# Performance work log

Measured on AMD Instinct MI355X. Metric: run time of the kernel, lower is better.

## Reference

```python
import jax, jax.numpy as jnp
import numpy as np

N, FIN, FOUT = 4096, 512, 256
ALPHA = 0.2          # LeakyReLU negative slope
NEG_INF = -9e15      # mask value from the torch source


def setup_inputs() -> dict:
    key = jax.random.key(0)
    ks = jax.random.split(key, 11)
    h = jax.random.normal(ks[0], (N, FIN), dtype=jnp.float32)
    adj_n = jax.random.randint(ks[1], (N, N), 0, 2, dtype=jnp.int32)
    adj_d = jax.random.randint(ks[2], (N, N), 0, 2, dtype=jnp.int32)
    G_nd = jax.random.normal(ks[3], (2, N, FOUT), dtype=jnp.float32)
    # learned parameters (xavier-ish scale)
    W_n = jax.random.normal(ks[4], (FIN, FOUT), dtype=jnp.float32) * 0.05
    a1_n = jax.random.normal(ks[5], (FOUT, 1), dtype=jnp.float32) * 0.05
    a2_n = jax.random.normal(ks[6], (FOUT, 1), dtype=jnp.float32) * 0.05
    W_d = jax.random.normal(ks[7], (FIN, FOUT), dtype=jnp.float32) * 0.05
    a1_d = jax.random.normal(ks[8], (FOUT, 1), dtype=jnp.float32) * 0.05
    a2_d = jax.random.normal(ks[9], (FOUT, 1), dtype=jnp.float32) * 0.05
    scale = jnp.zeros((1,), dtype=jnp.float32)
    return {"h": h, "adj_n": adj_n, "adj_d": adj_d, "G_nd": G_nd,
            "W_n": W_n, "a1_n": a1_n, "a2_n": a2_n,
            "W_d": W_d, "a1_d": a1_d, "a2_d": a2_d, "scale": scale}


def _gat(h, adj, W, a1, a2):
    # Wh: [N, FOUT]
    Wh = h @ W
    # outer-sum attention logits: e[i,j] = leakyrelu(Wh_i.a1 + Wh_j.a2)
    e = jax.nn.leaky_relu((Wh @ a1) + (Wh @ a2).T, negative_slope=ALPHA)  # [N, N]
    att = jnp.where(adj > 0, e, jnp.float32(NEG_INF))
    att = jax.nn.softmax(att, axis=-1)
    # dropout is identity in eval mode
    return jax.nn.elu(att @ Wh)  # [N, FOUT]


def reference(h, adj_n, adj_d, G_nd, W_n, a1_n, a2_n, W_d, a1_d, a2_d, scale):
    f_n_S = _gat(h, adj_n, W_n, a1_n, a2_n)
    f_d_S = _gat(h, adj_d, W_d, a1_d, a2_d)
    # The G_nd cross-attention branch (f_nd_C) in the torch source is computed
    # but never used in the returned value; omitted here (jit would DCE it).
    return f_n_S + f_d_S
```

## Files before the change

kernel.cpp:

```cpp
#include <hip/hip_runtime.h>

#define N_NODES 4096
#define FIN     512
#define FOUT    256

typedef __attribute__((ext_vector_type(8))) short bf16x8s;
typedef __attribute__((ext_vector_type(4))) float f32x4;
typedef __attribute__((ext_vector_type(8))) unsigned short u16x8;
typedef unsigned short u16;
typedef unsigned int   u32;

__device__ inline u16 f2b(float f) {
    union { float f; unsigned int u; } v; v.f = f;
    unsigned int r = v.u + 0x7fffu + ((v.u >> 16) & 1u);
    return (u16)(r >> 16);
}

__global__ __launch_bounds__(256) void prep_kernel(
    const float* __restrict__ h, const float* __restrict__ Wn,
    const float* __restrict__ Wd,
    u16* __restrict__ hb, u16* __restrict__ WTb, float* __restrict__ s12)
{
    __shared__ u16 tl[64 * 72];
    const int t = threadIdx.x;
    const int bid = blockIdx.x;

    if (bid < 1024) {
        int idx = (bid * 256 + t) * 8;
        float4 f0 = *(const float4*)&h[idx];
        float4 f1 = *(const float4*)&h[idx + 4];
        u16x8 o;
        o[0]=f2b(f0.x); o[1]=f2b(f0.y); o[2]=f2b(f0.z); o[3]=f2b(f0.w);
        o[4]=f2b(f1.x); o[5]=f2b(f1.y); o[6]=f2b(f1.z); o[7]=f2b(f1.w);
        *(u16x8*)&hb[idx] = o;
    } else if (bid < 1088) {
        int id = bid - 1024;
        int kx = id & 7, ny = (id >> 3) & 3, b = id >> 5;
        const float* W = b ? Wd : Wn;
        int k0 = kx * 64, n0 = ny * 64;
        int kr = t >> 2, nc0 = (t & 3) * 16;
        const float* src = W + (size_t)(k0 + kr) * FOUT + n0 + nc0;
        #pragma unroll
        for (int jv = 0; jv < 4; ++jv) {
            float4 f = *(const float4*)(src + jv * 4);
            tl[(nc0 + jv * 4 + 0) * 72 + kr] = f2b(f.x);
            tl[(nc0 + jv * 4 + 1) * 72 + kr] = f2b(f.y);
            tl[(nc0 + jv * 4 + 2) * 72 + kr] = f2b(f.z);
            tl[(nc0 + jv * 4 + 3) * 72 + kr] = f2b(f.w);
        }
        __syncthreads();
        int n = t >> 2, kc0 = (t & 3) * 16;
        u16* dst = WTb + ((size_t)b << 17) + (size_t)(n0 + n) * FIN + k0 + kc0;
        *(uint4*)dst       = *(uint4*)&tl[n * 72 + kc0];
        *(uint4*)(dst + 8) = *(uint4*)&tl[n * 72 + kc0 + 8];
    } else {
        float4 z = {0.f, 0.f, 0.f, 0.f};
        float4* p4 = (float4*)s12;
        #pragma unroll
        for (int k = 0; k < 16; ++k) p4[k * 256 + t] = z;
    }
}

__global__ __launch_bounds__(256) void wh_gemm_kernel(
    const u16* __restrict__ hb, const u16* __restrict__ WTb,
    const float* __restrict__ a1n, const float* __restrict__ a2n,
    const float* __restrict__ a1d, const float* __restrict__ a2d,
    u16* __restrict__ WhT, float* __restrict__ s1, float* __restrict__ s2)
{
    __shared__ u16 smem[8192];
    u16* a_lds = smem;
    u16* b_lds = smem + 4096;

    const int t = threadIdx.x, lane = t & 63, w = t >> 6;
    const int q = lane >> 4, ln = lane & 15;
    const int i0 = blockIdx.x * 64, n0 = blockIdx.y * 64, b = blockIdx.z;
    const u16* wt = WTb + ((size_t)b << 17);

    f32x4 acc[4];
    #pragma unroll
    for (int i = 0; i < 4; ++i) acc[i] = (f32x4){0.f, 0.f, 0.f, 0.f};

    for (int kt = 0; kt < 8; ++kt) {
        const int k0 = kt * 64;
        __syncthreads();
        #pragma unroll
        for (int it = 0; it < 2; ++it) {
            int chunk = it * 256 + t;
            int r = chunk >> 3, kc = chunk & 7;
            const u16* g = hb + (size_t)(i0 + r) * FIN + k0 + ((kc ^ (r & 7)) * 8);
            u16* l = a_lds + (it * 256 + w * 64) * 8;
            __builtin_amdgcn_global_load_lds(
                (const __attribute__((address_space(1))) void*)g,
                (__attribute__((address_space(3))) void*)l, 16, 0, 0);
        }
        #pragma unroll
        for (int it = 0; it < 2; ++it) {
            int chunk = it * 256 + t;
            int n = chunk >> 3, kc = chunk & 7;
            const u16* g = wt + (size_t)(n0 + n) * FIN + k0 + ((kc ^ (n & 7)) * 8);
            u16* l = b_lds + (it * 256 + w * 64) * 8;
            __builtin_amdgcn_global_load_lds(
                (const __attribute__((address_space(1))) void*)g,
                (__attribute__((address_space(3))) void*)l, 16, 0, 0);
        }
        __syncthreads();
        #pragma unroll
        for (int ks = 0; ks < 2; ++ks) {
            int sw = ((ks * 4 + q) ^ (ln & 7)) * 8;
            bf16x8s af = *(const bf16x8s*)&a_lds[(w * 16 + ln) * 64 + sw];
            #pragma unroll
            for (int nt = 0; nt < 4; ++nt) {
                bf16x8s bfv = *(const bf16x8s*)&b_lds[(nt * 16 + ln) * 64 + sw];
                acc[nt] = __builtin_amdgcn_mfma_f32_16x16x32_bf16(af, bfv, acc[nt], 0, 0, 0);
            }
        }
    }

    {
        const float* a1 = b ? a1d : a1n;
        const float* a2 = b ? a2d : a2n;
        float s1p[4] = {0.f, 0.f, 0.f, 0.f};
        float s2p[4] = {0.f, 0.f, 0.f, 0.f};
        #pragma unroll
        for (int nt = 0; nt < 4; ++nt) {
            float va1 = a1[n0 + nt * 16 + ln];
            float va2 = a2[n0 + nt * 16 + ln];
            #pragma unroll
            for (int r = 0; r < 4; ++r) {
                s1p[r] += acc[nt][r] * va1;
                s2p[r] += acc[nt][r] * va2;
            }
        }
        #pragma unroll
        for (int r = 0; r < 4; ++r) {
            #pragma unroll
            for (int off = 8; off >= 1; off >>= 1) {
                s1p[r] += __shfl_xor(s1p[r], off);
                s2p[r] += __shfl_xor(s2p[r], off);
            }
            if (ln == 0) {
                int row = i0 + w * 16 + q * 4 + r;
                atomicAdd(&s1[b * N_NODES + row], s1p[r]);
                atomicAdd(&s2[b * N_NODES + row], s2p[r]);
            }
        }
    }

    __syncthreads();
    #pragma unroll
    for (int nt = 0; nt < 4; ++nt)
        #pragma unroll
        for (int r = 0; r < 4; ++r)
            smem[(nt * 16 + ln) * 72 + (w * 16 + q * 4 + r)] = f2b(acc[nt][r]);
    __syncthreads();
    {
        const int nl = t >> 2, is = (t & 3) * 16;
        u16* dst = WhT + ((size_t)b << 20) + (size_t)(n0 + nl) * N_NODES + i0 + is;
        *(uint4*)dst       = *(uint4*)&smem[nl * 72 + is];
        *(uint4*)(dst + 8) = *(uint4*)&smem[nl * 72 + is + 8];
    }
}

__global__ __launch_bounds__(256) void attn_kernel(
    const int* __restrict__ adj_n, const int* __restrict__ adj_d,
    const u16* __restrict__ WhT,
    const float* __restrict__ s1, const float* __restrict__ s2,
    float* __restrict__ num_ws, float* __restrict__ den_ws, int nsplit)
{
    __shared__ u16 smem_all[20480];
    u16* wht_lds = smem_all;
    u16* p_lds   = smem_all + 16384;

    const int t = threadIdx.x, lane = t & 63, w = t >> 6;
    const int q = lane >> 4, ln = lane & 15;
    const int b = blockIdx.z, split = blockIdx.y;
    const int i0 = blockIdx.x * 64;
    const int jcount = N_NODES / nsplit;
    const int ntiles = jcount / 64;

    const int* adjb = b ? adj_d : adj_n;
    const u16* whtB = WhT + ((size_t)b << 20);
    const float* s1b = s1 + b * N_NODES;
    const float* s2b = s2 + b * N_NODES;

    const int pr = t >> 3;
    const int cw = t & 7;
    const int pc = cw * 8;
    const float s1v0 = s1b[i0 + pr];
    const float s1v1 = s1b[i0 + pr + 32];
    const size_t arow0 = (size_t)(i0 + pr) * N_NODES + pc;
    const size_t arow1 = arow0 + (size_t)32 * N_NODES;

    float den0 = 0.f, den1 = 0.f;

    f32x4 acc[4][4];
    #pragma unroll
    for (int mt = 0; mt < 4; ++mt)
        #pragma unroll
        for (int nt = 0; nt < 4; ++nt) acc[mt][nt] = (f32x4){0.f, 0.f, 0.f, 0.f};

    const int jbase = split * jcount;
    int4 a00_pf = *(const int4*)&adjb[arow0 + jbase];
    int4 a01_pf = *(const int4*)&adjb[arow0 + jbase + 4];
    int4 a10_pf = *(const int4*)&adjb[arow1 + jbase];
    int4 a11_pf = *(const int4*)&adjb[arow1 + jbase + 4];
    float4 sv0_pf = *(const float4*)&s2b[jbase + pc];
    float4 sv1_pf = *(const float4*)&s2b[jbase + pc + 4];

    for (int jt = 0; jt < ntiles; ++jt) {
        const int j0 = jbase + jt * 64;
        __syncthreads();
        #pragma unroll
        for (int it = 0; it < 8; ++it) {
            int chunk = it * 256 + t;
            int n = chunk >> 3, kc = chunk & 7;
            const u16* g = whtB + (size_t)n * N_NODES + j0 + ((kc ^ (n & 7)) * 8);
            u16* l = wht_lds + (it * 256 + w * 64) * 8;
            __builtin_amdgcn_global_load_lds(
                (const __attribute__((address_space(1))) void*)g,
                (__attribute__((address_space(3))) void*)l, 16, 0, 0);
        }
        int v0[8] = {a00_pf.x, a00_pf.y, a00_pf.z, a00_pf.w, a01_pf.x, a01_pf.y, a01_pf.z, a01_pf.w};
        int v1[8] = {a10_pf.x, a10_pf.y, a10_pf.z, a10_pf.w, a11_pf.x, a11_pf.y, a11_pf.z, a11_pf.w};
        float svf[8] = {sv0_pf.x, sv0_pf.y, sv0_pf.z, sv0_pf.w, sv1_pf.x, sv1_pf.y, sv1_pf.z, sv1_pf.w};
        u16x8 pk0, pk1;
        #pragma unroll
        for (int jj = 0; jj < 8; ++jj) {
            float sv = svf[jj];
            float x0 = s1v0 + sv, x1 = s1v1 + sv;
            float p0 = (v0[jj] > 0) ? __expf(fmaxf(x0, 0.2f * x0)) : 0.f;
            float p1 = (v1[jj] > 0) ? __expf(fmaxf(x1, 0.2f * x1)) : 0.f;
            den0 += p0; den1 += p1;
            pk0[jj] = f2b(p0); pk1[jj] = f2b(p1);
        }
        int swp = ((cw ^ (pr & 7)) * 8);
        *(u16x8*)&p_lds[pr * 64 + swp] = pk0;
        *(u16x8*)&p_lds[(pr + 32) * 64 + swp] = pk1;
        __syncthreads();
        if (jt + 1 < ntiles) {
            const int jn = j0 + 64;
            a00_pf = *(const int4*)&adjb[arow0 + jn];
            a01_pf = *(const int4*)&adjb[arow0 + jn + 4];
            a10_pf = *(const int4*)&adjb[arow1 + jn];
            a11_pf = *(const int4*)&adjb[arow1 + jn + 4];
            sv0_pf = *(const float4*)&s2b[jn + pc];
            sv1_pf = *(const float4*)&s2b[jn + pc + 4];
        }
        #pragma unroll
        for (int ks = 0; ks < 2; ++ks) {
            int sw = ((ks * 4 + q) ^ (ln & 7)) * 8;
            bf16x8s af[4];
            #pragma unroll
            for (int mt = 0; mt < 4; ++mt)
                af[mt] = *(const bf16x8s*)&p_lds[(mt * 16 + ln) * 64 + sw];
            #pragma unroll
            for (int nt = 0; nt < 4; ++nt) {
                bf16x8s bfv = *(const bf16x8s*)&wht_lds[(w * 64 + nt * 16 + ln) * 64 + sw];
                #pragma unroll
                for (int mt = 0; mt < 4; ++mt)
                    acc[mt][nt] = __builtin_amdgcn_mfma_f32_16x16x32_bf16(af[mt], bfv, acc[mt][nt], 0, 0, 0);
            }
        }
    }
    den0 += __shfl_down(den0, 4, 8); den1 += __shfl_down(den1, 4, 8);
    den0 += __shfl_down(den0, 2, 8); den1 += __shfl_down(den1, 2, 8);
    den0 += __shfl_down(den0, 1, 8); den1 += __shfl_down(den1, 1, 8);
    const size_t pbase = (size_t)(b * nsplit + split) * N_NODES;
    if ((t & 7) == 0) {
        den_ws[pbase + i0 + pr] = den0;
        den_ws[pbase + i0 + pr + 32] = den1;
    }
    #pragma unroll
    for (int mt = 0; mt < 4; ++mt)
        #pragma unroll
        for (int r = 0; r < 4; ++r) {
            int row = mt * 16 + q * 4 + r;
            #pragma unroll
            for (int nt = 0; nt < 4; ++nt)
                num_ws[(pbase + i0 + row) * FOUT + w * 64 + nt * 16 + ln] = acc[mt][nt][r];
        }
}

__global__ __launch_bounds__(256) void reduce_kernel(
    const float* __restrict__ num_ws, const float* __restrict__ den_ws,
    float* __restrict__ out, int nsplit)
{
    int gid = blockIdx.x * 256 + threadIdx.x;
    int i = gid >> 6;
    int f4 = (gid & 63) * 4;
    float4 o = {0.f, 0.f, 0.f, 0.f};
    #pragma unroll
    for (int b = 0; b < 2; ++b) {
        float4 num = {0.f, 0.f, 0.f, 0.f};
        float den = 0.f;
        for (int s = 0; s < nsplit; ++s) {
            const float4 v = *(const float4*)&num_ws[((size_t)(b * nsplit + s) * N_NODES + i) * FOUT + f4];
            num.x += v.x; num.y += v.y; num.z += v.z; num.w += v.w;
            den += den_ws[(size_t)(b * nsplit + s) * N_NODES + i];
        }
        float inv = 1.0f / den;
        float e0 = num.x * inv, e1 = num.y * inv, e2 = num.z * inv, e3 = num.w * inv;
        o.x += (e0 > 0.f) ? e0 : expm1f(e0);
        o.y += (e1 > 0.f) ? e1 : expm1f(e1);
        o.z += (e2 > 0.f) ? e2 : expm1f(e2);
        o.w += (e3 > 0.f) ? e3 : expm1f(e3);
    }
    *(float4*)&out[(size_t)i * FOUT + f4] = o;
}

extern "C" void kernel_launch(void* const* d_in, const int* in_sizes, int n_in,
                              void* d_out, int out_size, void* d_ws, size_t ws_size,
                              hipStream_t stream) {
    const float* h    = (const float*)d_in[0];
    const int*   adjn = (const int*)d_in[1];
    const int*   adjd = (const int*)d_in[2];
    const float* Wn   = (const float*)d_in[4];
    const float* a1n  = (const float*)d_in[5];
    const float* a2n  = (const float*)d_in[6];
    const float* Wd   = (const float*)d_in[7];
    const float* a1d  = (const float*)d_in[8];
    const float* a2d  = (const float*)d_in[9];

    char* ws = (char*)d_ws;
    u16*  WhT  = (u16*)ws;
    float* s1  = (float*)(ws + ((size_t)8 << 20));
    float* s2  = s1 + 2 * N_NODES;
    float* den = s2 + 2 * N_NODES;
    size_t num_off = ((size_t)8 << 20) + ((size_t)400 << 10);
    u16*  hb   = (u16*)(ws + num_off);
    u16*  WTb  = (u16*)(ws + num_off + ((size_t)4 << 20));
    float* num = (float*)(ws + num_off);

    const size_t per_split = (size_t)2 * N_NODES * FOUT * sizeof(float);
    int nsplit = (ws_size >= num_off + 8 * per_split) ? 8 : 4;

    prep_kernel<<<1089, 256, 0, stream>>>(h, Wn, Wd, hb, WTb, s1);
    wh_gemm_kernel<<<dim3(64, 4, 2), 256, 0, stream>>>(hb, WTb, a1n, a2n, a1d, a2d, WhT, s1, s2);
    attn_kernel<<<dim3(64, nsplit, 2), 256, 0, stream>>>(adjn, adjd, WhT, s1, s2, num, den, nsplit);
    reduce_kernel<<<1024, 256, 0, stream>>>(num, den, (float*)d_out, nsplit);
}
```

Before: 215.1 us.

## Double attention row tile to 128 rows and use nontemporal loads/stores

The attention kernel now handles 128 query rows per block instead of 64. Each WhT tile staged in LDS is reused across twice as many rows, which halves the WhT global traffic, and the grid shrinks from 64 to 32 blocks in x. Adjacency reads, num_ws stores and reduce_kernel loads now use nontemporal hints to avoid polluting the cache. In exchange, each thread holds twice as many accumulators, which raises register pressure, and the grid has half as many blocks (512 with 8 splits), which may leave CUs underused.

```diff
diff --git a/kernel.cpp b/kernel.cpp
--- a/kernel.cpp
+++ b/kernel.cpp
@@ -6,6 +6,7 @@
 
 typedef __attribute__((ext_vector_type(8))) short bf16x8s;
 typedef __attribute__((ext_vector_type(4))) float f32x4;
+typedef __attribute__((ext_vector_type(4))) int   i32x4;
 typedef __attribute__((ext_vector_type(8))) unsigned short u16x8;
 typedef unsigned short u16;
 typedef unsigned int   u32;
@@ -167,14 +168,13 @@
     const float* __restrict__ s1, const float* __restrict__ s2,
     float* __restrict__ num_ws, float* __restrict__ den_ws, int nsplit)
 {
-    __shared__ u16 smem_all[20480];
-    u16* wht_lds = smem_all;
-    u16* p_lds   = smem_all + 16384;
+    __shared__ u16 wht_lds[16384];
+    __shared__ u16 p_lds[8192];
 
     const int t = threadIdx.x, lane = t & 63, w = t >> 6;
     const int q = lane >> 4, ln = lane & 15;
     const int b = blockIdx.z, split = blockIdx.y;
-    const int i0 = blockIdx.x * 64;
+    const int i0 = blockIdx.x * 128;
     const int jcount = N_NODES / nsplit;
     const int ntiles = jcount / 64;
 
@@ -186,24 +186,29 @@
     const int pr = t >> 3;
     const int cw = t & 7;
     const int pc = cw * 8;
-    const float s1v0 = s1b[i0 + pr];
-    const float s1v1 = s1b[i0 + pr + 32];
-    const size_t arow0 = (size_t)(i0 + pr) * N_NODES + pc;
-    const size_t arow1 = arow0 + (size_t)32 * N_NODES;
-
-    float den0 = 0.f, den1 = 0.f;
-
-    f32x4 acc[4][4];
-    #pragma unroll
-    for (int mt = 0; mt < 4; ++mt)
+    float  s1v[4];
+    size_t arow[4];
+    #pragma unroll
+    for (int r = 0; r < 4; ++r) {
+        s1v[r]  = s1b[i0 + pr + 32 * r];
+        arow[r] = (size_t)(i0 + pr + 32 * r) * N_NODES + pc;
+    }
+
+    float den[4] = {0.f, 0.f, 0.f, 0.f};
+
+    f32x4 acc[8][4];
+    #pragma unroll
+    for (int mt = 0; mt < 8; ++mt)
         #pragma unroll
         for (int nt = 0; nt < 4; ++nt) acc[mt][nt] = (f32x4){0.f, 0.f, 0.f, 0.f};
 
     const int jbase = split * jcount;
-    int4 a00_pf = *(const int4*)&adjb[arow0 + jbase];
-    int4 a01_pf = *(const int4*)&adjb[arow0 + jbase + 4];
-    int4 a10_pf = *(const int4*)&adjb[arow1 + jbase];
-    int4 a11_pf = *(const int4*)&adjb[arow1 + jbase + 4];
+    i32x4 apf[4][2];
+    #pragma unroll
+    for (int r = 0; r < 4; ++r) {
+        apf[r][0] = __builtin_nontemporal_load((const i32x4*)&adjb[arow[r] + jbase]);
+        apf[r][1] = __builtin_nontemporal_load((const i32x4*)&adjb[arow[r] + jbase + 4]);
+    }
     float4 sv0_pf = *(const float4*)&s2b[jbase + pc];
     float4 sv1_pf = *(const float4*)&s2b[jbase + pc + 4];
 
@@ -220,64 +225,69 @@
                 (const __attribute__((address_space(1))) void*)g,
                 (__attribute__((address_space(3))) void*)l, 16, 0, 0);
         }
-        int v0[8] = {a00_pf.x, a00_pf.y, a00_pf.z, a00_pf.w, a01_pf.x, a01_pf.y, a01_pf.z, a01_pf.w};
-        int v1[8] = {a10_pf.x, a10_pf.y, a10_pf.z, a10_pf.w, a11_pf.x, a11_pf.y, a11_pf.z, a11_pf.w};
-        float svf[8] = {sv0_pf.x, sv0_pf.y, sv0_pf.z, sv0_pf.w, sv1_pf.x, sv1_pf.y, sv1_pf.z, sv1_pf.w};
-        u16x8 pk0, pk1;
-        #pragma unroll
-        for (int jj = 0; jj < 8; ++jj) {
-            float sv = svf[jj];
-            float x0 = s1v0 + sv, x1 = s1v1 + sv;
-            float p0 = (v0[jj] > 0) ? __expf(fmaxf(x0, 0.2f * x0)) : 0.f;
-            float p1 = (v1[jj] > 0) ? __expf(fmaxf(x1, 0.2f * x1)) : 0.f;
-            den0 += p0; den1 += p1;
-            pk0[jj] = f2b(p0); pk1[jj] = f2b(p1);
-        }
-        int swp = ((cw ^ (pr & 7)) * 8);
-        *(u16x8*)&p_lds[pr * 64 + swp] = pk0;
-        *(u16x8*)&p_lds[(pr + 32) * 64 + swp] = pk1;
+        float svf[8] = {sv0_pf.x, sv0_pf.y, sv0_pf.z, sv0_pf.w,
+                        sv1_pf.x, sv1_pf.y, sv1_pf.z, sv1_pf.w};
+        const int swp = ((cw ^ (pr & 7)) * 8);
+        #pragma unroll
+        for (int r = 0; r < 4; ++r) {
+            int v[8] = {apf[r][0][0], apf[r][0][1], apf[r][0][2], apf[r][0][3],
+                        apf[r][1][0], apf[r][1][1], apf[r][1][2], apf[r][1][3]};
+            u16x8 pk;
+            #pragma unroll
+            for (int jj = 0; jj < 8; ++jj) {
+                float x = s1v[r] + svf[jj];
+                float p = (v[jj] > 0) ? __expf(fmaxf(x, 0.2f * x)) : 0.f;
+                den[r] += p;
+                pk[jj] = f2b(p);
+            }
+            *(u16x8*)&p_lds[(pr + 32 * r) * 64 + swp] = pk;
+        }
         __syncthreads();
         if (jt + 1 < ntiles) {
             const int jn = j0 + 64;
-            a00_pf = *(const int4*)&adjb[arow0 + jn];
-            a01_pf = *(const int4*)&adjb[arow0 + jn + 4];
-            a10_pf = *(const int4*)&adjb[arow1 + jn];
-            a11_pf = *(const int4*)&adjb[arow1 + jn + 4];
+            #pragma unroll
+            for (int r = 0; r < 4; ++r) {
+                apf[r][0] = __builtin_nontemporal_load((const i32x4*)&adjb[arow[r] + jn]);
+                apf[r][1] = __builtin_nontemporal_load((const i32x4*)&adjb[arow[r] + jn + 4]);
+            }
             sv0_pf = *(const float4*)&s2b[jn + pc];
             sv1_pf = *(const float4*)&s2b[jn + pc + 4];
         }
         #pragma unroll
         for (int ks = 0; ks < 2; ++ks) {
             int sw = ((ks * 4 + q) ^ (ln & 7)) * 8;
-            bf16x8s af[4];
-            #pragma unroll
-            for (int mt = 0; mt < 4; ++mt)
-                af[mt] = *(const bf16x8s*)&p_lds[(mt * 16 + ln) * 64 + sw];
             #pragma unroll
             for (int nt = 0; nt < 4; ++nt) {
                 bf16x8s bfv = *(const bf16x8s*)&wht_lds[(w * 64 + nt * 16 + ln) * 64 + sw];
                 #pragma unroll
-                for (int mt = 0; mt < 4; ++mt)
-                    acc[mt][nt] = __builtin_amdgcn_mfma_f32_16x16x32_bf16(af[mt], bfv, acc[mt][nt], 0, 0, 0);
-            }
-        }
-    }
-    den0 += __shfl_down(den0, 4, 8); den1 += __shfl_down(den1, 4, 8);
-    den0 += __shfl_down(den0, 2, 8); den1 += __shfl_down(den1, 2, 8);
-    den0 += __shfl_down(den0, 1, 8); den1 += __shfl_down(den1, 1, 8);
+                for (int mt = 0; mt < 8; ++mt) {
+                    bf16x8s af = *(const bf16x8s*)&p_lds[(mt * 16 + ln) * 64 + sw];
+                    acc[mt][nt] = __builtin_amdgcn_mfma_f32_16x16x32_bf16(af, bfv, acc[mt][nt], 0, 0, 0);
+                }
+            }
+        }
+    }
+    #pragma unroll
+    for (int r = 0; r < 4; ++r) {
+        den[r] += __shfl_down(den[r], 4, 8);
+        den[r] += __shfl_down(den[r], 2, 8);
+        den[r] += __shfl_down(den[r], 1, 8);
+    }
     const size_t pbase = (size_t)(b * nsplit + split) * N_NODES;
     if ((t & 7) == 0) {
-        den_ws[pbase + i0 + pr] = den0;
-        den_ws[pbase + i0 + pr + 32] = den1;
-    }
-    #pragma unroll
-    for (int mt = 0; mt < 4; ++mt)
+        #pragma unroll
+        for (int r = 0; r < 4; ++r)
+            den_ws[pbase + i0 + pr + 32 * r] = den[r];
+    }
+    #pragma unroll
+    for (int mt = 0; mt < 8; ++mt)
         #pragma unroll
         for (int r = 0; r < 4; ++r) {
             int row = mt * 16 + q * 4 + r;
             #pragma unroll
             for (int nt = 0; nt < 4; ++nt)
-                num_ws[(pbase + i0 + row) * FOUT + w * 64 + nt * 16 + ln] = acc[mt][nt][r];
+                __builtin_nontemporal_store(acc[mt][nt][r],
+                    &num_ws[(pbase + i0 + row) * FOUT + w * 64 + nt * 16 + ln]);
         }
 }
 
@@ -294,8 +304,9 @@
         float4 num = {0.f, 0.f, 0.f, 0.f};
         float den = 0.f;
         for (int s = 0; s < nsplit; ++s) {
-            const float4 v = *(const float4*)&num_ws[((size_t)(b * nsplit + s) * N_NODES + i) * FOUT + f4];
-            num.x += v.x; num.y += v.y; num.z += v.z; num.w += v.w;
+            f32x4 v = __builtin_nontemporal_load(
+                (const f32x4*)&num_ws[((size_t)(b * nsplit + s) * N_NODES + i) * FOUT + f4]);
+            num.x += v[0]; num.y += v[1]; num.z += v[2]; num.w += v[3];
             den += den_ws[(size_t)(b * nsplit + s) * N_NODES + i];
         }
         float inv = 1.0f / den;
@@ -336,6 +347,6 @@
 
     prep_kernel<<<1089, 256, 0, stream>>>(h, Wn, Wd, hb, WTb, s1);
     wh_gemm_kernel<<<dim3(64, 4, 2), 256, 0, stream>>>(hb, WTb, a1n, a2n, a1d, a2d, WhT, s1, s2);
-    attn_kernel<<<dim3(64, nsplit, 2), 256, 0, stream>>>(adjn, adjd, WhT, s1, s2, num, den, nsplit);
+    attn_kernel<<<dim3(32, nsplit, 2), 256, 0, stream>>>(adjn, adjd, WhT, s1, s2, num, den, nsplit);
     reduce_kernel<<<1024, 256, 0, stream>>>(num, den, (float*)d_out, nsplit);
 }
```

New measurement: 224.7 us. +4.5%, slower.
